# Kernel optimization log

Hardware: AMD Instinct MI355X
Metric: run time of the kernel (lower is better)

The kernel has to match this reference:

```python
import jax, jax.numpy as jnp
import numpy as np

N = 100000
E = 1600000
IN_FT = 128
HID = 128
LEAK = 0.2  # GATConv default negative_slope


def _glorot(key, shape):
    fan_in, fan_out = shape[0], shape[-1]
    s = float(np.sqrt(6.0 / (fan_in + fan_out)))
    return jax.random.uniform(key, shape, jnp.float32, -s, s)


def setup_inputs() -> dict:
    key = jax.random.key(0)
    ks = jax.random.split(key, 12)
    return {
        "x": jax.random.normal(ks[0], (N, IN_FT), jnp.float32),
        "edge_index": jax.random.randint(ks[1], (2, E), 0, N, dtype=jnp.int64) if jax.config.jax_enable_x64 else jax.random.randint(ks[1], (2, E), 0, N, dtype=jnp.int32),
        "edge_weight": jax.random.uniform(ks[2], (E,), jnp.float32),
        "W1": _glorot(ks[3], (IN_FT, HID)),
        "a_src1": _glorot(ks[4], (HID, 1))[:, 0],
        "a_dst1": _glorot(ks[5], (HID, 1))[:, 0],
        "b1": jnp.zeros((HID,), jnp.float32),
        "W2": _glorot(ks[6], (HID, HID)),
        "a_src2": _glorot(ks[7], (HID, 1))[:, 0],
        "a_dst2": _glorot(ks[8], (HID, 1))[:, 0],
        "b2": jnp.zeros((HID,), jnp.float32),
    }


def _gat_layer(h_in, src, dst, n, W, a_src, a_dst, b):
    # h: [N, HID] dense projection
    h = h_in @ W
    # per-node attention halves, then edge-wise combine (classic GAT, 1 head)
    s_src = h @ a_src  # [N]
    s_dst = h @ a_dst  # [N]
    e = jax.nn.leaky_relu(s_src[src] + s_dst[dst], LEAK)  # [E+N]
    # softmax over incoming edges of each dst node (self-loops guarantee non-empty)
    m = jax.ops.segment_max(e, dst, num_segments=n)
    ex = jnp.exp(e - m[dst])
    denom = jax.ops.segment_sum(ex, dst, num_segments=n)
    alpha = ex / denom[dst]
    # scatter-aggregate messages alpha_ij * h_j
    out = jax.ops.segment_sum(alpha[:, None] * h[src], dst, num_segments=n)
    return out + b


def reference(x, edge_index, edge_weight, W1, a_src1, a_dst1, b1, W2, a_src2, a_dst2, b2):
    # edge_weight is accepted but unused: PyG GATConv with edge_dim=None ignores edge_attr.
    n = x.shape[0]
    loops = jnp.arange(n, dtype=edge_index.dtype)  # add_self_loops=True
    src = jnp.concatenate([edge_index[0], loops])
    dst = jnp.concatenate([edge_index[1], loops])
    x1 = jnp.tanh(_gat_layer(x, src, dst, n, W1, a_src1, a_dst1, b1))
    # dropout: identity in eval mode
    x2 = _gat_layer(x1, src, dst, n, W2, a_src2, a_dst2, b2)
    # update='max': elementwise max over stacked layer outputs
    return jnp.maximum(x1, x2)
```

## Files before the change

### kernel.cpp

```cpp
#include <hip/hip_runtime.h>
#include <math.h>

#define NN 100000
#define NE 1600000
#define EE 1700000
#define HD 128
#define NH (NN*HD)

#define BSH 8
#define NBUK 391
#define CAP 6144
#define EPB 4096
#define P1B ((EE + EPB - 1) / EPB)

typedef _Float16 f16x8 __attribute__((ext_vector_type(8)));
typedef _Float16 f16x4 __attribute__((ext_vector_type(4)));
typedef float    f32x4 __attribute__((ext_vector_type(4)));

__device__ __forceinline__ float fast_tanh(float x) {
    float e = __expf(2.f * x);
    return 1.f - 2.f * __builtin_amdgcn_rcpf(e + 1.f);
}

__launch_bounds__(256) __global__
void partition_kernel(const int* __restrict__ ei, int* __restrict__ bucketCount,
                      uint2* __restrict__ stage) {
    __shared__ int hist[NBUK];
    __shared__ int base[NBUK];
    int t = threadIdx.x;
    for (int i = t; i < NBUK; i += 256) hist[i] = 0;
    __syncthreads();
    int e0 = blockIdx.x * EPB;
    int e1 = min(e0 + EPB, EE);
    for (int e = e0 + t; e < e1; e += 256) {
        int d = (e < NE) ? ei[NE + e] : e - NE;
        atomicAdd(&hist[d >> BSH], 1);
    }
    __syncthreads();
    for (int i = t; i < NBUK; i += 256) {
        base[i] = atomicAdd(&bucketCount[i], hist[i]);
        hist[i] = 0;
    }
    __syncthreads();
    for (int e = e0 + t; e < e1; e += 256) {
        int s, d;
        if (e < NE) { s = ei[e]; d = ei[NE + e]; } else { s = e - NE; d = s; }
        int b = d >> BSH;
        int pos = base[b] + atomicAdd(&hist[b], 1);
        if (pos < CAP) stage[(size_t)b * CAP + pos] = make_uint2((unsigned)s, (unsigned)d);
    }
}

__global__ void bucket_scan_kernel(const int* __restrict__ bucketCount,
                                   int* __restrict__ bucketBase) {
    __shared__ int sd[512];
    int t = threadIdx.x;
    int v = (t < NBUK) ? bucketCount[t] : 0;
    sd[t] = v;
    __syncthreads();
    for (int off = 1; off < 512; off <<= 1) {
        int tmp = (t >= off) ? sd[t - off] : 0;
        __syncthreads();
        sd[t] += tmp;
        __syncthreads();
    }
    if (t < NBUK) bucketBase[t] = sd[t] - v;
}

__launch_bounds__(256) __global__
void bucket_build_kernel(const uint2* __restrict__ stage, const int* __restrict__ bucketCount,
                         const int* __restrict__ bucketBase, int* __restrict__ row_ptr,
                         int* __restrict__ csr_src) {
    int b = blockIdx.x;
    int t = threadIdx.x;
    __shared__ int ldeg[256];
    __shared__ int loff[256];
    ldeg[t] = 0;
    __syncthreads();
    int cnt  = bucketCount[b];
    int base = bucketBase[b];
    const uint2* sp = stage + (size_t)b * CAP;
    int n0 = b << BSH;
    for (int i = t; i < cnt; i += 256) {
        uint2 p = sp[i];
        atomicAdd(&ldeg[p.y - n0], 1);
    }
    __syncthreads();
    int v = ldeg[t];
    loff[t] = v;
    __syncthreads();
    for (int off = 1; off < 256; off <<= 1) {
        int tmp = (t >= off) ? loff[t - off] : 0;
        __syncthreads();
        loff[t] += tmp;
        __syncthreads();
    }
    int excl = loff[t] - v;
    int n = n0 + t;
    if (n < NN) row_ptr[n] = base + excl;
    if (b == NBUK - 1 && t == 0) row_ptr[NN] = EE;
    ldeg[t] = excl;
    __syncthreads();
    for (int i = t; i < cnt; i += 256) {
        uint2 p = sp[i];
        int lp = atomicAdd(&ldeg[p.y - n0], 1);
        csr_src[base + lp] = (int)p.x;
    }
}

__global__ void wt_kernel(const float* __restrict__ W, _Float16* __restrict__ Wt) {
    int e = blockIdx.x * 256 + threadIdx.x;
    int k = e >> 7, n = e & 127;
    Wt[n*HD + k] = (_Float16)W[e];
}

__launch_bounds__(256) __global__
void gemm16_kernel(const float* __restrict__ A, const _Float16* __restrict__ Wt,
                   _Float16* __restrict__ H, const float* __restrict__ a_src,
                   const float* __restrict__ a_dst, float* __restrict__ s_src,
                   float* __restrict__ s_dst) {
    __shared__ __align__(16) _Float16 Wl[HD*HD];
    __shared__ float asl[HD], adl[HD];
    int t = threadIdx.x;
    #pragma unroll
    for (int i = 0; i < 8; ++i) {
        int f = t + 256*i;
        int n = f >> 4, slot = f & 15;
        int phys = n*16 + (slot ^ (n & 7));
        *(float4*)(Wl + (size_t)phys*8) = ((const float4*)Wt)[f];
    }
    if (t < HD) { asl[t] = a_src[t]; adl[t] = a_dst[t]; }
    __syncthreads();

    int wave = t >> 6, lane = t & 63;
    int row0 = blockIdx.x*64 + wave*16;
    int h8   = lane >> 4;
    int col  = lane & 15;
    int arow = row0 + col; if (arow >= NN) arow = NN - 1;
    const float* Af = A + (size_t)arow*HD + h8*8;

    f32x4 acc[8];
    #pragma unroll
    for (int i = 0; i < 8; ++i) acc[i] = (f32x4){0.f,0.f,0.f,0.f};

    #pragma unroll
    for (int step = 0; step < 4; ++step) {
        float4 fa = *(const float4*)(Af + step*32);
        float4 fb = *(const float4*)(Af + step*32 + 4);
        f16x8 a = { (_Float16)fa.x, (_Float16)fa.y, (_Float16)fa.z, (_Float16)fa.w,
                    (_Float16)fb.x, (_Float16)fb.y, (_Float16)fb.z, (_Float16)fb.w };
        #pragma unroll
        for (int nt = 0; nt < 8; ++nt) {
            int n = nt*16 + col;
            int slot = step*4 + h8;
            f16x8 bfr = *(const f16x8*)(Wl + (size_t)(n*16 + (slot ^ (n & 7)))*8);
            acc[nt] = __builtin_amdgcn_mfma_f32_16x16x32_f16(a, bfr, acc[nt], 0, 0, 0);
        }
    }

    int orow0 = row0 + h8*4;
    #pragma unroll
    for (int nt = 0; nt < 8; ++nt) {
        int c = nt*16 + col;
        #pragma unroll
        for (int r = 0; r < 4; ++r) {
            int row = orow0 + r;
            if (row < NN) H[(size_t)row*HD + c] = (_Float16)acc[nt][r];
        }
    }

    float pS[4] = {0.f,0.f,0.f,0.f}, pD[4] = {0.f,0.f,0.f,0.f};
    #pragma unroll
    for (int nt = 0; nt < 8; ++nt) {
        float as_ = asl[nt*16 + col], ad_ = adl[nt*16 + col];
        #pragma unroll
        for (int r = 0; r < 4; ++r) {
            pS[r] += acc[nt][r] * as_;
            pD[r] += acc[nt][r] * ad_;
        }
    }
    #pragma unroll
    for (int off = 1; off < 16; off <<= 1) {
        #pragma unroll
        for (int r = 0; r < 4; ++r) {
            pS[r] += __shfl_xor(pS[r], off);
            pD[r] += __shfl_xor(pD[r], off);
        }
    }
    if (col == 0) {
        #pragma unroll
        for (int r = 0; r < 4; ++r) {
            int row = orow0 + r;
            if (row < NN) { s_src[row] = pS[r]; s_dst[row] = pD[r]; }
        }
    }
}

template<int LAYER>
__launch_bounds__(256) __global__
void gat_node_kernel(const int* __restrict__ row_ptr, const int* __restrict__ csr_src,
                     const float* __restrict__ s_src, const float* __restrict__ s_dst,
                     const _Float16* __restrict__ Hh, const float* __restrict__ bias,
                     float* __restrict__ out) {
    int wid = (blockIdx.x * blockDim.x + threadIdx.x) >> 6;
    int lane = threadIdx.x & 63;
    int g = lane >> 4, l16 = lane & 15;
    int n = wid*4 + g;
    if (n >= NN) return;
    int r0 = row_ptr[n], r1 = row_ptr[n+1];
    float sdv = s_dst[n];
    int last = r1 - 1;

    float denom = 0.f;
    float acc[8] = {0.f,0.f,0.f,0.f,0.f,0.f,0.f,0.f};

    for (int j = r0; j < r1; j += 4) {
        int jB = j+1 <= last ? j+1 : last;
        int jC = j+2 <= last ? j+2 : last;
        int jD = j+3 <= last ? j+3 : last;
        int sA = csr_src[j];
        int sB = csr_src[jB];
        int sC = csr_src[jC];
        int sD = csr_src[jD];
        f16x8 hA = *(const f16x8*)(Hh + (unsigned)(sA << 7) + l16*8);
        f16x8 hB = *(const f16x8*)(Hh + (unsigned)(sB << 7) + l16*8);
        f16x8 hC = *(const f16x8*)(Hh + (unsigned)(sC << 7) + l16*8);
        f16x8 hD = *(const f16x8*)(Hh + (unsigned)(sD << 7) + l16*8);
        float eA = s_src[sA] + sdv;
        float eB = s_src[sB] + sdv;
        float eC = s_src[sC] + sdv;
        float eD = s_src[sD] + sdv;
        eA = eA > 0.f ? eA : 0.2f*eA;  eB = eB > 0.f ? eB : 0.2f*eB;
        eC = eC > 0.f ? eC : 0.2f*eC;  eD = eD > 0.f ? eD : 0.2f*eD;
        float wA = __expf(fminf(eA, 80.f));
        float wB = (j+1 < r1) ? __expf(fminf(eB, 80.f)) : 0.f;
        float wC = (j+2 < r1) ? __expf(fminf(eC, 80.f)) : 0.f;
        float wD = (j+3 < r1) ? __expf(fminf(eD, 80.f)) : 0.f;
        denom += (wA + wB) + (wC + wD);
        #pragma unroll
        for (int i = 0; i < 8; ++i)
            acc[i] += wA*(float)hA[i] + wB*(float)hB[i] + wC*(float)hC[i] + wD*(float)hD[i];
    }

    float inv = __builtin_amdgcn_rcpf(denom);
    float* op = out + (unsigned)(n << 7) + l16*8;
    float4 b0 = *(const float4*)(bias + l16*8);
    float4 b1 = *(const float4*)(bias + l16*8 + 4);
    float r[8];
    r[0]=acc[0]*inv+b0.x; r[1]=acc[1]*inv+b0.y; r[2]=acc[2]*inv+b0.z; r[3]=acc[3]*inv+b0.w;
    r[4]=acc[4]*inv+b1.x; r[5]=acc[5]*inv+b1.y; r[6]=acc[6]*inv+b1.z; r[7]=acc[7]*inv+b1.w;
    if (LAYER == 1) {
        #pragma unroll
        for (int i = 0; i < 8; ++i) r[i] = fast_tanh(r[i]);
    } else {
        float4 x0 = *(const float4*)op;
        float4 x1 = *(const float4*)(op + 4);
        r[0]=fmaxf(x0.x,r[0]); r[1]=fmaxf(x0.y,r[1]); r[2]=fmaxf(x0.z,r[2]); r[3]=fmaxf(x0.w,r[3]);
        r[4]=fmaxf(x1.x,r[4]); r[5]=fmaxf(x1.y,r[5]); r[6]=fmaxf(x1.z,r[6]); r[7]=fmaxf(x1.w,r[7]);
    }
    *(float4*)op       = make_float4(r[0],r[1],r[2],r[3]);
    *(float4*)(op + 4) = make_float4(r[4],r[5],r[6],r[7]);
}

extern "C" void kernel_launch(void* const* d_in, const int* in_sizes, int n_in,
                              void* d_out, int out_size, void* d_ws, size_t ws_size,
                              hipStream_t stream) {
    const float* x   = (const float*)d_in[0];
    const int*   ei  = (const int*)d_in[1];
    const float* W1  = (const float*)d_in[3];
    const float* as1 = (const float*)d_in[4];
    const float* ad1 = (const float*)d_in[5];
    const float* b1  = (const float*)d_in[6];
    const float* W2  = (const float*)d_in[7];
    const float* as2 = (const float*)d_in[8];
    const float* ad2 = (const float*)d_in[9];
    const float* b2  = (const float*)d_in[10];
    float* out = (float*)d_out;

    char* wsb = (char*)d_ws;
    _Float16* h  = (_Float16*)wsb;
    _Float16* Wt = h + NH;
    float* ssrc  = (float*)(wsb + (size_t)NH*2 + 32768);
    float* sdst  = ssrc + NN;
    int* row_ptr = (int*)(sdst + NN);
    int* csr_src = row_ptr + NN + 2;
    int* bucketCount = csr_src + EE;
    int* bucketBase  = bucketCount + NBUK;
    uint2* stage = (uint2*)(bucketBase + NBUK + 2);

    dim3 B(256);
    int gemm_blocks = (NN + 63) / 64;
    int node_blocks = NN / 16;

    hipMemsetAsync(bucketCount, 0, NBUK * sizeof(int), stream);
    partition_kernel<<<P1B, B, 0, stream>>>(ei, bucketCount, stage);
    bucket_scan_kernel<<<1, 512, 0, stream>>>(bucketCount, bucketBase);
    bucket_build_kernel<<<NBUK, B, 0, stream>>>(stage, bucketCount, bucketBase, row_ptr, csr_src);

    wt_kernel<<<64, B, 0, stream>>>(W1, Wt);
    gemm16_kernel<<<gemm_blocks, B, 0, stream>>>(x, Wt, h, as1, ad1, ssrc, sdst);
    gat_node_kernel<1><<<node_blocks, B, 0, stream>>>(row_ptr, csr_src, ssrc, sdst, h, b1, out);

    wt_kernel<<<64, B, 0, stream>>>(W2, Wt);
    gemm16_kernel<<<gemm_blocks, B, 0, stream>>>(out, Wt, h, as2, ad2, ssrc, sdst);
    gat_node_kernel<2><<<node_blocks, B, 0, stream>>>(row_ptr, csr_src, ssrc, sdst, h, b2, out);
}
```

Baseline: 238.1 us.

## Fuse GEMM with edge partition, pack stage entries, degree-sort nodes, prefetch gathers

Several ideas land together. The layer-1 GEMM and the edge-bucket partition now run in one launch so their blocks overlap. The bucket scan kernel is folded into bucket_build, the two weight transposes share one launch, and stage entries shrink from 8 bytes to a 4-byte packed word. A degree histogram and a new permutation kernel order nodes by in-degree so the 16-lane node groups in a wave have similar trip counts. The aggregation loop also software-pipelines its gathers. This trades extra launches and indirection through perm for less launch overhead, less staging traffic, better load balance and more latency hiding.

```diff
diff --git a/kernel.cpp b/kernel.cpp
--- a/kernel.cpp
+++ b/kernel.cpp
@@ -12,9 +12,9 @@
 #define CAP 6144
 #define EPB 4096
 #define P1B ((EE + EPB - 1) / EPB)
+#define GEMMB 1563
 
 typedef _Float16 f16x8 __attribute__((ext_vector_type(8)));
-typedef _Float16 f16x4 __attribute__((ext_vector_type(4)));
 typedef float    f32x4 __attribute__((ext_vector_type(4)));
 
 __device__ __forceinline__ float fast_tanh(float x) {
@@ -22,71 +22,161 @@
     return 1.f - 2.f * __builtin_amdgcn_rcpf(e + 1.f);
 }
 
+__global__ void wt12_kernel(const float* __restrict__ W1, const float* __restrict__ W2,
+                            _Float16* __restrict__ Wt1, _Float16* __restrict__ Wt2) {
+    int b = blockIdx.x;
+    const float* W = (b < 64) ? W1 : W2;
+    _Float16* Wt   = (b < 64) ? Wt1 : Wt2;
+    int e = (b & 63) * 256 + threadIdx.x;
+    int k = e >> 7, n = e & 127;
+    Wt[n*HD + k] = (_Float16)W[e];
+}
+
 __launch_bounds__(256) __global__
-void partition_kernel(const int* __restrict__ ei, int* __restrict__ bucketCount,
-                      uint2* __restrict__ stage) {
-    __shared__ int hist[NBUK];
-    __shared__ int base[NBUK];
+void gemm_part_kernel(const float* __restrict__ A, const _Float16* __restrict__ Wt,
+                      _Float16* __restrict__ H, const float* __restrict__ a_src,
+                      const float* __restrict__ a_dst, float* __restrict__ s_src,
+                      float* __restrict__ s_dst,
+                      const int* __restrict__ ei, int* __restrict__ bucketCount,
+                      unsigned* __restrict__ stage) {
+    __shared__ __align__(16) char smem[HD*HD*2 + HD*8];
+    int bid = blockIdx.x;
     int t = threadIdx.x;
-    for (int i = t; i < NBUK; i += 256) hist[i] = 0;
-    __syncthreads();
-    int e0 = blockIdx.x * EPB;
-    int e1 = min(e0 + EPB, EE);
-    for (int e = e0 + t; e < e1; e += 256) {
-        int d = (e < NE) ? ei[NE + e] : e - NE;
-        atomicAdd(&hist[d >> BSH], 1);
-    }
-    __syncthreads();
-    for (int i = t; i < NBUK; i += 256) {
-        base[i] = atomicAdd(&bucketCount[i], hist[i]);
-        hist[i] = 0;
-    }
-    __syncthreads();
-    for (int e = e0 + t; e < e1; e += 256) {
-        int s, d;
-        if (e < NE) { s = ei[e]; d = ei[NE + e]; } else { s = e - NE; d = s; }
-        int b = d >> BSH;
-        int pos = base[b] + atomicAdd(&hist[b], 1);
-        if (pos < CAP) stage[(size_t)b * CAP + pos] = make_uint2((unsigned)s, (unsigned)d);
-    }
-}
-
-__global__ void bucket_scan_kernel(const int* __restrict__ bucketCount,
-                                   int* __restrict__ bucketBase) {
-    __shared__ int sd[512];
-    int t = threadIdx.x;
-    int v = (t < NBUK) ? bucketCount[t] : 0;
-    sd[t] = v;
-    __syncthreads();
-    for (int off = 1; off < 512; off <<= 1) {
-        int tmp = (t >= off) ? sd[t - off] : 0;
-        __syncthreads();
-        sd[t] += tmp;
-        __syncthreads();
-    }
-    if (t < NBUK) bucketBase[t] = sd[t] - v;
+
+    if (bid < GEMMB) {
+        _Float16* Wl = (_Float16*)smem;
+        float* asl = (float*)(smem + HD*HD*2);
+        float* adl = asl + HD;
+        #pragma unroll
+        for (int i = 0; i < 8; ++i) {
+            int f = t + 256*i;
+            int n = f >> 4, slot = f & 15;
+            int phys = n*16 + (slot ^ (n & 7));
+            *(float4*)(Wl + (size_t)phys*8) = ((const float4*)Wt)[f];
+        }
+        if (t < HD) { asl[t] = a_src[t]; adl[t] = a_dst[t]; }
+        __syncthreads();
+
+        int wave = t >> 6, lane = t & 63;
+        int row0 = bid*64 + wave*16;
+        int h8   = lane >> 4;
+        int col  = lane & 15;
+        int arow = row0 + col; if (arow >= NN) arow = NN - 1;
+        const float* Af = A + (size_t)arow*HD + h8*8;
+
+        f32x4 acc[8];
+        #pragma unroll
+        for (int i = 0; i < 8; ++i) acc[i] = (f32x4){0.f,0.f,0.f,0.f};
+
+        #pragma unroll
+        for (int step = 0; step < 4; ++step) {
+            float4 fa = *(const float4*)(Af + step*32);
+            float4 fb = *(const float4*)(Af + step*32 + 4);
+            f16x8 a = { (_Float16)fa.x, (_Float16)fa.y, (_Float16)fa.z, (_Float16)fa.w,
+                        (_Float16)fb.x, (_Float16)fb.y, (_Float16)fb.z, (_Float16)fb.w };
+            #pragma unroll
+            for (int nt = 0; nt < 8; ++nt) {
+                int n = nt*16 + col;
+                int slot = step*4 + h8;
+                f16x8 bfr = *(const f16x8*)(Wl + (size_t)(n*16 + (slot ^ (n & 7)))*8);
+                acc[nt] = __builtin_amdgcn_mfma_f32_16x16x32_f16(a, bfr, acc[nt], 0, 0, 0);
+            }
+        }
+
+        int orow0 = row0 + h8*4;
+        #pragma unroll
+        for (int nt = 0; nt < 8; ++nt) {
+            int c = nt*16 + col;
+            #pragma unroll
+            for (int r = 0; r < 4; ++r) {
+                int row = orow0 + r;
+                if (row < NN) H[(size_t)row*HD + c] = (_Float16)acc[nt][r];
+            }
+        }
+
+        float pS[4] = {0.f,0.f,0.f,0.f}, pD[4] = {0.f,0.f,0.f,0.f};
+        #pragma unroll
+        for (int nt = 0; nt < 8; ++nt) {
+            float as_ = asl[nt*16 + col], ad_ = adl[nt*16 + col];
+            #pragma unroll
+            for (int r = 0; r < 4; ++r) { pS[r] += acc[nt][r]*as_; pD[r] += acc[nt][r]*ad_; }
+        }
+        #pragma unroll
+        for (int off = 1; off < 16; off <<= 1) {
+            #pragma unroll
+            for (int r = 0; r < 4; ++r) {
+                pS[r] += __shfl_xor(pS[r], off);
+                pD[r] += __shfl_xor(pD[r], off);
+            }
+        }
+        if (col == 0) {
+            #pragma unroll
+            for (int r = 0; r < 4; ++r) {
+                int row = orow0 + r;
+                if (row < NN) { s_src[row] = pS[r]; s_dst[row] = pD[r]; }
+            }
+        }
+    } else if (ei) {
+        int* hist = (int*)smem;
+        int* base = hist + NBUK;
+        for (int i = t; i < NBUK; i += 256) hist[i] = 0;
+        __syncthreads();
+        int pb = bid - GEMMB;
+        int e0 = pb * EPB;
+        int e1 = min(e0 + EPB, EE);
+        for (int e = e0 + t; e < e1; e += 256) {
+            int d = (e < NE) ? ei[NE + e] : e - NE;
+            atomicAdd(&hist[d >> BSH], 1);
+        }
+        __syncthreads();
+        for (int i = t; i < NBUK; i += 256) {
+            base[i] = atomicAdd(&bucketCount[i], hist[i]);
+            hist[i] = 0;
+        }
+        __syncthreads();
+        for (int e = e0 + t; e < e1; e += 256) {
+            int s, d;
+            if (e < NE) { s = ei[e]; d = ei[NE + e]; } else { s = e - NE; d = s; }
+            int b = d >> BSH;
+            int pos = base[b] + atomicAdd(&hist[b], 1);
+            if (pos < CAP)
+                stage[(size_t)b * CAP + pos] = (unsigned)s | ((unsigned)(d & 255) << 20);
+        }
+    }
 }
 
 __launch_bounds__(256) __global__
-void bucket_build_kernel(const uint2* __restrict__ stage, const int* __restrict__ bucketCount,
-                         const int* __restrict__ bucketBase, int* __restrict__ row_ptr,
-                         int* __restrict__ csr_src) {
+void bucket_build_kernel(const unsigned* __restrict__ stage, const int* __restrict__ bucketCount,
+                         int* __restrict__ row_ptr, int* __restrict__ csr_src,
+                         int* __restrict__ degCount) {
     int b = blockIdx.x;
     int t = threadIdx.x;
     __shared__ int ldeg[256];
     __shared__ int loff[256];
+    __shared__ int dhist[64];
+    __shared__ int sbase;
+    int c = 0;
+    if (t < b) c = bucketCount[t];
+    if (t + 256 < b) c += bucketCount[t + 256];
+    loff[t] = c;
     ldeg[t] = 0;
+    if (t < 64) dhist[t] = 0;
+    __syncthreads();
+    for (int off = 128; off >= 1; off >>= 1) {
+        if (t < off) loff[t] += loff[t + off];
+        __syncthreads();
+    }
+    if (t == 0) sbase = loff[0];
     __syncthreads();
     int cnt  = bucketCount[b];
-    int base = bucketBase[b];
-    const uint2* sp = stage + (size_t)b * CAP;
+    int base = sbase;
+    const unsigned* sp = stage + (size_t)b * CAP;
     int n0 = b << BSH;
-    for (int i = t; i < cnt; i += 256) {
-        uint2 p = sp[i];
-        atomicAdd(&ldeg[p.y - n0], 1);
-    }
+    for (int i = t; i < cnt; i += 256) atomicAdd(&ldeg[sp[i] >> 20], 1);
     __syncthreads();
     int v = ldeg[t];
+    int n = n0 + t;
+    if (n < NN) atomicAdd(&dhist[min(v, 63)], 1);
     loff[t] = v;
     __syncthreads();
     for (int off = 1; off < 256; off <<= 1) {
@@ -96,140 +186,83 @@
         __syncthreads();
     }
     int excl = loff[t] - v;
-    int n = n0 + t;
     if (n < NN) row_ptr[n] = base + excl;
     if (b == NBUK - 1 && t == 0) row_ptr[NN] = EE;
+    if (t < 64 && dhist[t]) atomicAdd(&degCount[t], dhist[t]);
     ldeg[t] = excl;
     __syncthreads();
     for (int i = t; i < cnt; i += 256) {
-        uint2 p = sp[i];
-        int lp = atomicAdd(&ldeg[p.y - n0], 1);
-        csr_src[base + lp] = (int)p.x;
-    }
-}
-
-__global__ void wt_kernel(const float* __restrict__ W, _Float16* __restrict__ Wt) {
-    int e = blockIdx.x * 256 + threadIdx.x;
-    int k = e >> 7, n = e & 127;
-    Wt[n*HD + k] = (_Float16)W[e];
+        unsigned p = sp[i];
+        int lp = atomicAdd(&ldeg[p >> 20], 1);
+        csr_src[base + lp] = (int)(p & 0xFFFFFu);
+    }
 }
 
 __launch_bounds__(256) __global__
-void gemm16_kernel(const float* __restrict__ A, const _Float16* __restrict__ Wt,
-                   _Float16* __restrict__ H, const float* __restrict__ a_src,
-                   const float* __restrict__ a_dst, float* __restrict__ s_src,
-                   float* __restrict__ s_dst) {
-    __shared__ __align__(16) _Float16 Wl[HD*HD];
-    __shared__ float asl[HD], adl[HD];
-    int t = threadIdx.x;
-    #pragma unroll
-    for (int i = 0; i < 8; ++i) {
-        int f = t + 256*i;
-        int n = f >> 4, slot = f & 15;
-        int phys = n*16 + (slot ^ (n & 7));
-        *(float4*)(Wl + (size_t)phys*8) = ((const float4*)Wt)[f];
-    }
-    if (t < HD) { asl[t] = a_src[t]; adl[t] = a_dst[t]; }
-    __syncthreads();
-
-    int wave = t >> 6, lane = t & 63;
-    int row0 = blockIdx.x*64 + wave*16;
-    int h8   = lane >> 4;
-    int col  = lane & 15;
-    int arow = row0 + col; if (arow >= NN) arow = NN - 1;
-    const float* Af = A + (size_t)arow*HD + h8*8;
-
-    f32x4 acc[8];
-    #pragma unroll
-    for (int i = 0; i < 8; ++i) acc[i] = (f32x4){0.f,0.f,0.f,0.f};
-
-    #pragma unroll
-    for (int step = 0; step < 4; ++step) {
-        float4 fa = *(const float4*)(Af + step*32);
-        float4 fb = *(const float4*)(Af + step*32 + 4);
-        f16x8 a = { (_Float16)fa.x, (_Float16)fa.y, (_Float16)fa.z, (_Float16)fa.w,
-                    (_Float16)fb.x, (_Float16)fb.y, (_Float16)fb.z, (_Float16)fb.w };
-        #pragma unroll
-        for (int nt = 0; nt < 8; ++nt) {
-            int n = nt*16 + col;
-            int slot = step*4 + h8;
-            f16x8 bfr = *(const f16x8*)(Wl + (size_t)(n*16 + (slot ^ (n & 7)))*8);
-            acc[nt] = __builtin_amdgcn_mfma_f32_16x16x32_f16(a, bfr, acc[nt], 0, 0, 0);
-        }
-    }
-
-    int orow0 = row0 + h8*4;
-    #pragma unroll
-    for (int nt = 0; nt < 8; ++nt) {
-        int c = nt*16 + col;
-        #pragma unroll
-        for (int r = 0; r < 4; ++r) {
-            int row = orow0 + r;
-            if (row < NN) H[(size_t)row*HD + c] = (_Float16)acc[nt][r];
-        }
-    }
-
-    float pS[4] = {0.f,0.f,0.f,0.f}, pD[4] = {0.f,0.f,0.f,0.f};
-    #pragma unroll
-    for (int nt = 0; nt < 8; ++nt) {
-        float as_ = asl[nt*16 + col], ad_ = adl[nt*16 + col];
-        #pragma unroll
-        for (int r = 0; r < 4; ++r) {
-            pS[r] += acc[nt][r] * as_;
-            pD[r] += acc[nt][r] * ad_;
-        }
-    }
-    #pragma unroll
-    for (int off = 1; off < 16; off <<= 1) {
-        #pragma unroll
-        for (int r = 0; r < 4; ++r) {
-            pS[r] += __shfl_xor(pS[r], off);
-            pD[r] += __shfl_xor(pD[r], off);
-        }
-    }
-    if (col == 0) {
-        #pragma unroll
-        for (int r = 0; r < 4; ++r) {
-            int row = orow0 + r;
-            if (row < NN) { s_src[row] = pS[r]; s_dst[row] = pD[r]; }
-        }
-    }
+void perm_kernel(const int* __restrict__ row_ptr, const int* __restrict__ degCount,
+                 int* __restrict__ degCursor, int* __restrict__ perm) {
+    __shared__ int dbase[64], lhist[64], lbase[64];
+    int t = threadIdx.x, n = blockIdx.x * 256 + t;
+    if (t < 64) lhist[t] = 0;
+    __syncthreads();
+    int d = 0, myt = 0;
+    if (n < NN) {
+        int deg = row_ptr[n+1] - row_ptr[n];
+        d = min(deg, 63);
+        myt = atomicAdd(&lhist[d], 1);
+    }
+    __syncthreads();
+    if (t < 64) lbase[t] = lhist[t] ? atomicAdd(&degCursor[t], lhist[t]) : 0;
+    if (t == 0) {
+        int run = 0;
+        for (int i = 0; i < 64; ++i) { dbase[i] = run; run += degCount[i]; }
+    }
+    __syncthreads();
+    if (n < NN) perm[dbase[d] + lbase[d] + myt] = n;
 }
 
 template<int LAYER>
 __launch_bounds__(256) __global__
-void gat_node_kernel(const int* __restrict__ row_ptr, const int* __restrict__ csr_src,
+void gat_node_kernel(const int* __restrict__ perm, const int* __restrict__ row_ptr,
+                     const int* __restrict__ csr_src,
                      const float* __restrict__ s_src, const float* __restrict__ s_dst,
                      const _Float16* __restrict__ Hh, const float* __restrict__ bias,
                      float* __restrict__ out) {
     int wid = (blockIdx.x * blockDim.x + threadIdx.x) >> 6;
     int lane = threadIdx.x & 63;
     int g = lane >> 4, l16 = lane & 15;
-    int n = wid*4 + g;
-    if (n >= NN) return;
+    int idx = wid*4 + g;
+    if (idx >= NN) return;
+    int n = perm[idx];
     int r0 = row_ptr[n], r1 = row_ptr[n+1];
+    int last = r1 - 1;
     float sdv = s_dst[n];
-    int last = r1 - 1;
 
     float denom = 0.f;
     float acc[8] = {0.f,0.f,0.f,0.f,0.f,0.f,0.f,0.f};
 
-    for (int j = r0; j < r1; j += 4) {
-        int jB = j+1 <= last ? j+1 : last;
-        int jC = j+2 <= last ? j+2 : last;
-        int jD = j+3 <= last ? j+3 : last;
-        int sA = csr_src[j];
-        int sB = csr_src[jB];
-        int sC = csr_src[jC];
-        int sD = csr_src[jD];
-        f16x8 hA = *(const f16x8*)(Hh + (unsigned)(sA << 7) + l16*8);
-        f16x8 hB = *(const f16x8*)(Hh + (unsigned)(sB << 7) + l16*8);
-        f16x8 hC = *(const f16x8*)(Hh + (unsigned)(sC << 7) + l16*8);
-        f16x8 hD = *(const f16x8*)(Hh + (unsigned)(sD << 7) + l16*8);
-        float eA = s_src[sA] + sdv;
-        float eB = s_src[sB] + sdv;
-        float eC = s_src[sC] + sdv;
-        float eD = s_src[sD] + sdv;
+    int j = r0;
+    int jB = min(j+1, last), jC = min(j+2, last), jD = min(j+3, last);
+    int sA = csr_src[j],  sB = csr_src[jB], sC = csr_src[jC], sD = csr_src[jD];
+    f16x8 hA = *(const f16x8*)(Hh + (unsigned)(sA << 7) + l16*8);
+    f16x8 hB = *(const f16x8*)(Hh + (unsigned)(sB << 7) + l16*8);
+    f16x8 hC = *(const f16x8*)(Hh + (unsigned)(sC << 7) + l16*8);
+    f16x8 hD = *(const f16x8*)(Hh + (unsigned)(sD << 7) + l16*8);
+    float vA = s_src[sA], vB = s_src[sB], vC = s_src[sC], vD = s_src[sD];
+
+    while (true) {
+        int jn = j + 4;
+        bool more = jn < r1;
+        int kj = more ? jn : r0;
+        int kB = min(kj+1, last), kC = min(kj+2, last), kD = min(kj+3, last);
+        int tA = csr_src[kj], tB = csr_src[kB], tC = csr_src[kC], tD = csr_src[kD];
+        f16x8 nA = *(const f16x8*)(Hh + (unsigned)(tA << 7) + l16*8);
+        f16x8 nB = *(const f16x8*)(Hh + (unsigned)(tB << 7) + l16*8);
+        f16x8 nC = *(const f16x8*)(Hh + (unsigned)(tC << 7) + l16*8);
+        f16x8 nD = *(const f16x8*)(Hh + (unsigned)(tD << 7) + l16*8);
+        float uA = s_src[tA], uB = s_src[tB], uC = s_src[tC], uD = s_src[tD];
+
+        float eA = vA + sdv, eB = vB + sdv, eC = vC + sdv, eD = vD + sdv;
         eA = eA > 0.f ? eA : 0.2f*eA;  eB = eB > 0.f ? eB : 0.2f*eB;
         eC = eC > 0.f ? eC : 0.2f*eC;  eD = eD > 0.f ? eD : 0.2f*eD;
         float wA = __expf(fminf(eA, 80.f));
@@ -240,6 +273,12 @@
         #pragma unroll
         for (int i = 0; i < 8; ++i)
             acc[i] += wA*(float)hA[i] + wB*(float)hB[i] + wC*(float)hC[i] + wD*(float)hD[i];
+
+        if (!more) break;
+        j = jn;
+        sA = tA; sB = tB; sC = tC; sD = tD;
+        hA = nA; hB = nB; hC = nC; hD = nD;
+        vA = uA; vB = uB; vC = uC; vD = uD;
     }
 
     float inv = __builtin_amdgcn_rcpf(denom);
@@ -278,30 +317,33 @@
     float* out = (float*)d_out;
 
     char* wsb = (char*)d_ws;
-    _Float16* h  = (_Float16*)wsb;
-    _Float16* Wt = h + NH;
-    float* ssrc  = (float*)(wsb + (size_t)NH*2 + 32768);
-    float* sdst  = ssrc + NN;
-    int* row_ptr = (int*)(sdst + NN);
-    int* csr_src = row_ptr + NN + 2;
+    _Float16* h   = (_Float16*)wsb;
+    _Float16* Wt1 = h + NH;
+    _Float16* Wt2 = Wt1 + HD*HD;
+    float* ssrc   = (float*)(Wt2 + HD*HD);
+    float* sdst   = ssrc + NN;
+    int* row_ptr  = (int*)(sdst + NN);
+    int* perm     = row_ptr + NN + 2;
+    int* csr_src  = perm + NN;
     int* bucketCount = csr_src + EE;
-    int* bucketBase  = bucketCount + NBUK;
-    uint2* stage = (uint2*)(bucketBase + NBUK + 2);
+    int* degCount    = bucketCount + NBUK;
+    int* degCursor   = degCount + 64;
+    unsigned* stage  = (unsigned*)(degCursor + 64 + 2);
 
     dim3 B(256);
-    int gemm_blocks = (NN + 63) / 64;
     int node_blocks = NN / 16;
 
-    hipMemsetAsync(bucketCount, 0, NBUK * sizeof(int), stream);
-    partition_kernel<<<P1B, B, 0, stream>>>(ei, bucketCount, stage);
-    bucket_scan_kernel<<<1, 512, 0, stream>>>(bucketCount, bucketBase);
-    bucket_build_kernel<<<NBUK, B, 0, stream>>>(stage, bucketCount, bucketBase, row_ptr, csr_src);
-
-    wt_kernel<<<64, B, 0, stream>>>(W1, Wt);
-    gemm16_kernel<<<gemm_blocks, B, 0, stream>>>(x, Wt, h, as1, ad1, ssrc, sdst);
-    gat_node_kernel<1><<<node_blocks, B, 0, stream>>>(row_ptr, csr_src, ssrc, sdst, h, b1, out);
-
-    wt_kernel<<<64, B, 0, stream>>>(W2, Wt);
-    gemm16_kernel<<<gemm_blocks, B, 0, stream>>>(out, Wt, h, as2, ad2, ssrc, sdst);
-    gat_node_kernel<2><<<node_blocks, B, 0, stream>>>(row_ptr, csr_src, ssrc, sdst, h, b2, out);
-}
+    hipMemsetAsync(bucketCount, 0, (NBUK + 128) * sizeof(int), stream);
+    wt12_kernel<<<128, B, 0, stream>>>(W1, W2, Wt1, Wt2);
+
+    gemm_part_kernel<<<GEMMB + P1B, B, 0, stream>>>(x, Wt1, h, as1, ad1, ssrc, sdst,
+                                                    ei, bucketCount, stage);
+    bucket_build_kernel<<<NBUK, B, 0, stream>>>(stage, bucketCount, row_ptr, csr_src, degCount);
+    perm_kernel<<<NBUK, B, 0, stream>>>(row_ptr, degCount, degCursor, perm);
+
+    gat_node_kernel<1><<<node_blocks, B, 0, stream>>>(perm, row_ptr, csr_src, ssrc, sdst, h, b1, out);
+
+    gemm_part_kernel<<<GEMMB, B, 0, stream>>>(out, Wt2, h, as2, ad2, ssrc, sdst,
+                                              nullptr, nullptr, nullptr);
+    gat_node_kernel<2><<<node_blocks, B, 0, stream>>>(perm, row_ptr, csr_src, ssrc, sdst, h, b2, out);
+}
```

New measurement: 267.1 us. 12.2% more time.
